# Optimization experiments

Hardware: AMD Instinct MI355X
Metric: run time of the kernel (lower is better)

## Reference

```python
import jax, jax.numpy as jnp
import numpy as np

EMBEDDING_DIM = 256
NUM_EMBEDDINGS = 2048
COMMITMENT_COST = 0.25


def setup_inputs() -> dict:
    key = jax.random.key(0)
    k1, k2 = jax.random.split(key)
    inputs = jax.random.normal(k1, (32, EMBEDDING_DIM, 32, 32), dtype=jnp.float32)
    # learned codebook buffer, shape (D, K) as in the torch module
    embedding = jax.random.normal(k2, (EMBEDDING_DIM, NUM_EMBEDDINGS), dtype=jnp.float32)
    return {"inputs": inputs, "embedding": embedding}


def reference(inputs, embedding):
    # Eval-mode forward of VectorQuantizerEMA (EMA buffer updates are
    # training-only side effects and do not affect the returned values).
    B, D, H, W = inputs.shape
    K = embedding.shape[1]
    x = inputs.astype(jnp.float32)
    # (B, D, H, W) -> (N, D), N = B*H*W, clamped as in the source
    flat = jnp.clip(jnp.transpose(x, (0, 2, 3, 1)).reshape(-1, D), -10.0, 10.0)
    # squared L2 distances to every codeword: (N, K)
    distances = (
        jnp.sum(flat * flat, axis=1, keepdims=True)
        + jnp.sum(embedding * embedding, axis=0, keepdims=True)
        - 2.0 * (flat @ embedding)
    )
    encoding_indices = jnp.argmin(distances, axis=1)  # (N,)
    # one-hot @ emb.T is just a gather of codebook columns
    q_flat = jnp.take(embedding.T, encoding_indices, axis=0)  # (N, D)
    quantized = jnp.transpose(q_flat.reshape(B, H, W, D), (0, 3, 1, 2))
    # VQ losses (computed against the un-clamped float inputs, as in torch)
    e_latent_loss = jnp.mean((jax.lax.stop_gradient(quantized) - x) ** 2)
    q_latent_loss = jnp.mean((quantized - jax.lax.stop_gradient(x)) ** 2)
    loss = q_latent_loss + COMMITMENT_COST * e_latent_loss
    # straight-through estimator
    quantized_st = inputs + jax.lax.stop_gradient(quantized - inputs)
    # perplexity from codeword usage (mean one-hot == normalized counts)
    n = encoding_indices.shape[0]
    avg_probs = jnp.zeros((K,), dtype=jnp.float32).at[encoding_indices].add(1.0) / n
    perplexity = jnp.exp(-jnp.sum(avg_probs * jnp.log(avg_probs + 1e-10)))
    return quantized_st, loss, perplexity, encoding_indices
```

## Files before the change

kernel.cpp:

```cpp
#include <hip/hip_runtime.h>
#include <hip/hip_bf16.h>
#include <math.h>

typedef unsigned int  uint;
typedef unsigned short ushort;

#define DD    256
#define KK    2048
#define HW    1024
#define NN    32768
#define NUMEL 8388608
#define STRIDEB (DD*HW)
#define NBLK_QL (NUMEL/1024)

#define WS_H2     0
#define WS_COUNTS 8192
#define WS_LOSS   16384
#define WS_EBF    16512
#define WS_PV     2113664
#define WS_PI     2375808
#define WS_BPART  WS_PV

#define OUT_LOSS  8388608
#define OUT_PPL   8388609
#define OUT_IDX   8388610

typedef __attribute__((ext_vector_type(8))) short  short8;
typedef __attribute__((ext_vector_type(4))) float  float4v;

__device__ __forceinline__ ushort f2bf(float f) {
    uint u = __float_as_uint(f);
    return (ushort)((u + 0x7FFFu + ((u >> 16) & 1u)) >> 16);
}

__global__ __launch_bounds__(256) void e2h_kernel(const float* __restrict__ emb,
                                                  float* __restrict__ h2,
                                                  int*   __restrict__ counts) {
    int k = blockIdx.x * 256 + threadIdx.x;
    float s = 0.f;
    for (int d = 0; d < DD; ++d) {
        float v = emb[(size_t)d * KK + k];
        s += v * v;
    }
    h2[k] = 0.5f * s;
    counts[k] = 0;
}

__global__ __launch_bounds__(256) void prep_emb(const float* __restrict__ emb,
                                                ushort* __restrict__ ebf) {
    int g  = blockIdx.x * 256 + threadIdx.x;
    int k  = g & (KK - 1);
    int dg = g >> 11;
    int d0 = dg * 8;
    int s    = dg >> 2;
    int quad = dg & 3;
    int ct   = k >> 4;
    int l    = quad * 16 + (k & 15);

    union { ushort us[8]; uint4 v; } hu, lu;
#pragma unroll
    for (int j = 0; j < 8; ++j) {
        float v = emb[(size_t)(d0 + j) * KK + k];
        ushort hb = f2bf(v);
        float  hf = __uint_as_float(((uint)hb) << 16);
        hu.us[j] = hb;
        lu.us[j] = f2bf(v - hf);
    }
    size_t hi_off = (size_t)(((ct * 8 + s) * 2 + 0) * 64 + l) * 8;
    size_t lo_off = (size_t)(((ct * 8 + s) * 2 + 1) * 64 + l) * 8;
    *(uint4*)(ebf + hi_off) = hu.v;
    *(uint4*)(ebf + lo_off) = lu.v;
}

__global__ __launch_bounds__(256, 2) void argmin_mfma(
    const float*  __restrict__ x,
    const ushort* __restrict__ ebf,
    const float*  __restrict__ h2,
    float* __restrict__ pv,
    int*   __restrict__ pi)
{
    __shared__ ushort sB[16384];
    __shared__ float  sH[1024];

    const int tid  = threadIdx.x;
    const int w    = tid >> 6;
    const int lane = tid & 63;
    const int m    = lane & 15;
    const int quad = lane >> 4;

    const int rb = blockIdx.x >> 1;
    const int ch = blockIdx.x & 1;
    const int n0 = rb * 128 + w * 32;
    const int b  = n0 >> 10;
    const int hwb = n0 & 1023;
    const float* xb = x + (size_t)b * STRIDEB;
    const int cbase = ch * 1024;
    const int ctg0  = cbase >> 4;

    auto stage = [&](int bufsel, int ctg) {
        const char* gb = (const char*)ebf + (size_t)ctg * 16384;
        char* lb = (char*)sB + (bufsel << 14);
#pragma unroll
        for (int i = 0; i < 4; ++i) {
            const int chunk = (w * 4 + i) << 10;
            __builtin_amdgcn_global_load_lds(
                (const __attribute__((address_space(1))) uint*)(gb + chunk + lane * 16),
                (__attribute__((address_space(3))) uint*)(lb + chunk),
                16, 0, 0);
        }
    };

    ((float4*)sH)[tid] = ((const float4*)(h2 + cbase))[tid];
    stage(0, ctg0);

    short8 xh[2][8], xl[2][8];
#pragma unroll
    for (int st = 0; st < 2; ++st) {
        const int hw = hwb + st * 16 + m;
#pragma unroll
        for (int s = 0; s < 8; ++s) {
            const float* p = xb + (size_t)(s * 32 + quad * 8) * HW + hw;
            short8 hh, ll;
#pragma unroll
            for (int j = 0; j < 8; ++j) {
                float v = p[(size_t)j * HW];
                v = fminf(fmaxf(v, -10.f), 10.f);
                ushort hb = f2bf(v);
                float  hf = __uint_as_float(((uint)hb) << 16);
                hh[j] = (short)hb;
                ll[j] = (short)f2bf(v - hf);
            }
            xh[st][s] = hh;
            xl[st][s] = ll;
        }
    }

    float bv[2][4] = {{1e30f,1e30f,1e30f,1e30f},{1e30f,1e30f,1e30f,1e30f}};
    int   bi[2][4] = {{0,0,0,0},{0,0,0,0}};

    for (int ct = 0; ct < 64; ++ct) {
        __syncthreads();
        if (ct < 63) stage((ct + 1) & 1, ctg0 + ct + 1);

        const ushort* bufc = sB + ((ct & 1) << 13);
        float4v ahh0 = {0,0,0,0}, ahl0 = {0,0,0,0}, alh0 = {0,0,0,0};
        float4v ahh1 = {0,0,0,0}, ahl1 = {0,0,0,0}, alh1 = {0,0,0,0};
#pragma unroll
        for (int s = 0; s < 8; ++s) {
            short8 eh = *(const short8*)&bufc[(s * 2 + 0) * 512 + lane * 8];
            short8 el = *(const short8*)&bufc[(s * 2 + 1) * 512 + lane * 8];
            alh0 = __builtin_amdgcn_mfma_f32_16x16x32_bf16(xl[0][s], eh, alh0, 0, 0, 0);
            ahl0 = __builtin_amdgcn_mfma_f32_16x16x32_bf16(xh[0][s], el, ahl0, 0, 0, 0);
            ahh0 = __builtin_amdgcn_mfma_f32_16x16x32_bf16(xh[0][s], eh, ahh0, 0, 0, 0);
            alh1 = __builtin_amdgcn_mfma_f32_16x16x32_bf16(xl[1][s], eh, alh1, 0, 0, 0);
            ahl1 = __builtin_amdgcn_mfma_f32_16x16x32_bf16(xh[1][s], el, ahl1, 0, 0, 0);
            ahh1 = __builtin_amdgcn_mfma_f32_16x16x32_bf16(xh[1][s], eh, ahh1, 0, 0, 0);
        }
        const int c  = cbase + ct * 16 + m;
        const float hv = sH[ct * 16 + m];
#pragma unroll
        for (int i = 0; i < 4; ++i) {
            float s0 = hv - (ahh0[i] + (ahl0[i] + alh0[i]));
            float s1 = hv - (ahh1[i] + (ahl1[i] + alh1[i]));
            if (s0 < bv[0][i]) { bv[0][i] = s0; bi[0][i] = c; }
            if (s1 < bv[1][i]) { bv[1][i] = s1; bi[1][i] = c; }
        }
    }

#pragma unroll
    for (int st = 0; st < 2; ++st) {
#pragma unroll
        for (int i = 0; i < 4; ++i) {
            float v  = bv[st][i];
            int   ix = bi[st][i];
#pragma unroll
            for (int msk = 8; msk >= 1; msk >>= 1) {
                float ov = __shfl_xor(v, msk, 64);
                int   oi = __shfl_xor(ix, msk, 64);
                if (ov < v || (ov == v && oi < ix)) { v = ov; ix = oi; }
            }
            if (m == 0) {
                int n = n0 + st * 16 + quad * 4 + i;
                pv[n * 2 + ch] = v;
                pi[n * 2 + ch] = ix;
            }
        }
    }
}

__global__ __launch_bounds__(256) void merge_kernel(
    const float* __restrict__ pv, const int* __restrict__ pi,
    float* __restrict__ out_idx_f, int* __restrict__ counts)
{
    int n = blockIdx.x * 256 + threadIdx.x;
    float v0 = pv[n * 2 + 0], v1 = pv[n * 2 + 1];
    int   i0 = pi[n * 2 + 0], i1 = pi[n * 2 + 1];
    int ix = (v1 < v0) ? i1 : i0;
    ix = min(max(ix, 0), KK - 1);
    out_idx_f[n] = (float)ix;
    atomicAdd(&counts[ix], 1);
}

__global__ __launch_bounds__(256) void quant_loss_kernel(
    const float* __restrict__ x,
    const float* __restrict__ emb,
    const float* __restrict__ idxf,
    float* __restrict__ outq,
    float* __restrict__ bpart)
{
    __shared__ float red[4];
    size_t o4 = ((size_t)blockIdx.x * 256 + threadIdx.x) * 4;
    int b  = (int)(o4 >> 18);
    int d  = (int)((o4 >> 10) & 255);
    int n  = b * HW + (int)(o4 & 1023);
    int i0 = (int)idxf[n + 0];
    int i1 = (int)idxf[n + 1];
    int i2 = (int)idxf[n + 2];
    int i3 = (int)idxf[n + 3];
    i0 = min(max(i0, 0), KK - 1); i1 = min(max(i1, 0), KK - 1);
    i2 = min(max(i2, 0), KK - 1); i3 = min(max(i3, 0), KK - 1);
    const float* er = emb + (size_t)d * KK;
    float4 q;
    q.x = er[i0]; q.y = er[i1]; q.z = er[i2]; q.w = er[i3];
    const float4 xv = *(const float4*)(x + o4);
    *(float4*)(outq + o4) = q;
    float ax = q.x - xv.x, ay = q.y - xv.y, az = q.z - xv.z, aw = q.w - xv.w;
    float s = ax * ax + ay * ay + az * az + aw * aw;
#pragma unroll
    for (int off = 32; off > 0; off >>= 1) s += __shfl_down(s, off, 64);
    if ((threadIdx.x & 63) == 0) red[threadIdx.x >> 6] = s;
    __syncthreads();
    if (threadIdx.x == 0)
        bpart[blockIdx.x] = red[0] + red[1] + red[2] + red[3];
}

__global__ __launch_bounds__(256) void finalize_kernel(
    const int* __restrict__ counts,
    const float* __restrict__ bpart,
    float* __restrict__ out)
{
    __shared__ float redp[4], redl[4];
    int tid = threadIdx.x;
    float s = 0.f;
    for (int k = tid; k < KK; k += 256) {
        float p = (float)counts[k] * (1.0f / (float)NN);
        s += p * logf(p + 1e-10f);
    }
    float ls = 0.f;
    for (int k = tid; k < NBLK_QL; k += 256) ls += bpart[k];
#pragma unroll
    for (int off = 32; off > 0; off >>= 1) {
        s  += __shfl_down(s, off, 64);
        ls += __shfl_down(ls, off, 64);
    }
    if ((tid & 63) == 0) { redp[tid >> 6] = s; redl[tid >> 6] = ls; }
    __syncthreads();
    if (tid == 0) {
        float tot = redp[0] + redp[1] + redp[2] + redp[3];
        float lsum = redl[0] + redl[1] + redl[2] + redl[3];
        out[OUT_PPL]  = expf(-tot);
        out[OUT_LOSS] = lsum * 1.25f / (float)NUMEL;
    }
}

extern "C" void kernel_launch(void* const* d_in, const int* in_sizes, int n_in,
                              void* d_out, int out_size, void* d_ws, size_t ws_size,
                              hipStream_t stream) {
    const float* x   = (const float*)d_in[0];
    const float* emb = (const float*)d_in[1];
    float* out = (float*)d_out;
    char*  ws  = (char*)d_ws;

    float*  h2     = (float*)(ws + WS_H2);
    int*    counts = (int*)(ws + WS_COUNTS);
    ushort* ebf    = (ushort*)(ws + WS_EBF);
    float*  pv     = (float*)(ws + WS_PV);
    int*    pi     = (int*)(ws + WS_PI);
    float*  bpart  = (float*)(ws + WS_BPART);

    e2h_kernel<<<KK / 256, 256, 0, stream>>>(emb, h2, counts);
    prep_emb<<<256, 256, 0, stream>>>(emb, ebf);
    argmin_mfma<<<512, 256, 0, stream>>>(x, ebf, h2, pv, pi);
    merge_kernel<<<NN / 256, 256, 0, stream>>>(pv, pi, out + OUT_IDX, counts);
    quant_loss_kernel<<<NBLK_QL, 256, 0, stream>>>(x, emb, out + OUT_IDX, out, bpart);
    finalize_kernel<<<1, 256, 0, stream>>>(counts, bpart, out);
}
```

Baseline: 233.6 us.

## Split codebook search four ways and merge partial argmins with packed 64-bit atomicMin

The argmin kernel now divides the 2048 codewords into four 512-wide chunks instead of two, doubling the grid to 1024 blocks and raising the launch-bounds occupancy hint to 4 blocks per CU. Partial (distance, index) results are packed into an order-preserving 64-bit key and combined with atomicMin into a buffer initialised by the norm kernel, which replaces the separate value/index arrays. The aim is better CU fill and latency hiding. The cost is that each block reloads and converts its x tile to bf16 hi/lo twice as often, and it adds global atomic traffic plus register pressure under the tighter bound. Ties still resolve to the lower index.

```diff
diff --git a/kernel.cpp b/kernel.cpp
--- a/kernel.cpp
+++ b/kernel.cpp
@@ -4,6 +4,7 @@
 
 typedef unsigned int  uint;
 typedef unsigned short ushort;
+typedef unsigned long long u64;
 
 #define DD    256
 #define KK    2048
@@ -15,11 +16,9 @@
 
 #define WS_H2     0
 #define WS_COUNTS 8192
-#define WS_LOSS   16384
 #define WS_EBF    16512
-#define WS_PV     2113664
-#define WS_PI     2375808
-#define WS_BPART  WS_PV
+#define WS_PACK   2113664
+#define WS_BPART  WS_PACK
 
 #define OUT_LOSS  8388608
 #define OUT_PPL   8388609
@@ -35,7 +34,8 @@
 
 __global__ __launch_bounds__(256) void e2h_kernel(const float* __restrict__ emb,
                                                   float* __restrict__ h2,
-                                                  int*   __restrict__ counts) {
+                                                  int*   __restrict__ counts,
+                                                  u64*   __restrict__ pack) {
     int k = blockIdx.x * 256 + threadIdx.x;
     float s = 0.f;
     for (int d = 0; d < DD; ++d) {
@@ -44,6 +44,8 @@
     }
     h2[k] = 0.5f * s;
     counts[k] = 0;
+#pragma unroll
+    for (int i = 0; i < 16; ++i) pack[k * 16 + i] = ~0ull;
 }
 
 __global__ __launch_bounds__(256) void prep_emb(const float* __restrict__ emb,
@@ -72,15 +74,14 @@
     *(uint4*)(ebf + lo_off) = lu.v;
 }
 
-__global__ __launch_bounds__(256, 2) void argmin_mfma(
+__global__ __launch_bounds__(256, 4) void argmin_mfma(
     const float*  __restrict__ x,
     const ushort* __restrict__ ebf,
     const float*  __restrict__ h2,
-    float* __restrict__ pv,
-    int*   __restrict__ pi)
+    u64*  __restrict__ pack)
 {
     __shared__ ushort sB[16384];
-    __shared__ float  sH[1024];
+    __shared__ float  sH[512];
 
     const int tid  = threadIdx.x;
     const int w    = tid >> 6;
@@ -88,13 +89,13 @@
     const int m    = lane & 15;
     const int quad = lane >> 4;
 
-    const int rb = blockIdx.x >> 1;
-    const int ch = blockIdx.x & 1;
+    const int rb = blockIdx.x >> 2;
+    const int ch = blockIdx.x & 3;
     const int n0 = rb * 128 + w * 32;
     const int b  = n0 >> 10;
     const int hwb = n0 & 1023;
     const float* xb = x + (size_t)b * STRIDEB;
-    const int cbase = ch * 1024;
+    const int cbase = ch * 512;
     const int ctg0  = cbase >> 4;
 
     auto stage = [&](int bufsel, int ctg) {
@@ -110,7 +111,7 @@
         }
     };
 
-    ((float4*)sH)[tid] = ((const float4*)(h2 + cbase))[tid];
+    if (tid < 128) ((float4*)sH)[tid] = ((const float4*)(h2 + cbase))[tid];
     stage(0, ctg0);
 
     short8 xh[2][8], xl[2][8];
@@ -138,9 +139,9 @@
     float bv[2][4] = {{1e30f,1e30f,1e30f,1e30f},{1e30f,1e30f,1e30f,1e30f}};
     int   bi[2][4] = {{0,0,0,0},{0,0,0,0}};
 
-    for (int ct = 0; ct < 64; ++ct) {
+    for (int ct = 0; ct < 32; ++ct) {
         __syncthreads();
-        if (ct < 63) stage((ct + 1) & 1, ctg0 + ct + 1);
+        if (ct < 31) stage((ct + 1) & 1, ctg0 + ct + 1);
 
         const ushort* bufc = sB + ((ct & 1) << 13);
         float4v ahh0 = {0,0,0,0}, ahl0 = {0,0,0,0}, alh0 = {0,0,0,0};
@@ -181,21 +182,21 @@
             }
             if (m == 0) {
                 int n = n0 + st * 16 + quad * 4 + i;
-                pv[n * 2 + ch] = v;
-                pi[n * 2 + ch] = ix;
+                uint u  = __float_as_uint(v);
+                uint mm = (u & 0x80000000u) ? ~u : (u | 0x80000000u);
+                u64 packed = ((u64)mm << 32) | (uint)ix;
+                atomicMin(&pack[n], packed);
             }
         }
     }
 }
 
 __global__ __launch_bounds__(256) void merge_kernel(
-    const float* __restrict__ pv, const int* __restrict__ pi,
+    const u64* __restrict__ pack,
     float* __restrict__ out_idx_f, int* __restrict__ counts)
 {
     int n = blockIdx.x * 256 + threadIdx.x;
-    float v0 = pv[n * 2 + 0], v1 = pv[n * 2 + 1];
-    int   i0 = pi[n * 2 + 0], i1 = pi[n * 2 + 1];
-    int ix = (v1 < v0) ? i1 : i0;
+    int ix = (int)(pack[n] & 0xFFFFFFFFull);
     ix = min(max(ix, 0), KK - 1);
     out_idx_f[n] = (float)ix;
     atomicAdd(&counts[ix], 1);
@@ -274,14 +275,13 @@
     float*  h2     = (float*)(ws + WS_H2);
     int*    counts = (int*)(ws + WS_COUNTS);
     ushort* ebf    = (ushort*)(ws + WS_EBF);
-    float*  pv     = (float*)(ws + WS_PV);
-    int*    pi     = (int*)(ws + WS_PI);
+    u64*    pack   = (u64*)(ws + WS_PACK);
     float*  bpart  = (float*)(ws + WS_BPART);
 
-    e2h_kernel<<<KK / 256, 256, 0, stream>>>(emb, h2, counts);
+    e2h_kernel<<<KK / 256, 256, 0, stream>>>(emb, h2, counts, pack);
     prep_emb<<<256, 256, 0, stream>>>(emb, ebf);
-    argmin_mfma<<<512, 256, 0, stream>>>(x, ebf, h2, pv, pi);
-    merge_kernel<<<NN / 256, 256, 0, stream>>>(pv, pi, out + OUT_IDX, counts);
+    argmin_mfma<<<1024, 256, 0, stream>>>(x, ebf, h2, pack);
+    merge_kernel<<<NN / 256, 256, 0, stream>>>(pack, out + OUT_IDX, counts);
     quant_loss_kernel<<<NBLK_QL, 256, 0, stream>>>(x, emb, out + OUT_IDX, out, bpart);
     finalize_kernel<<<1, 256, 0, stream>>>(counts, bpart, out);
 }
```

After: 527.3 us. +125.7%, slower.
